# Kernel tuning notes

Hardware: AMD Instinct MI355X
Metric: run time of the kernel (lower is better)

## Reference

```python
import jax, jax.numpy as jnp
import numpy as np

N_NODES = 100000
N_EDGES = 1600000
IN_DIM = 128
HID = 128
OUT_DIM = 1
EPS = 1e-5
NEG_SLOPE = 0.01


def _glorot(key, shape):
    fan_in = shape[-1]
    return jax.random.normal(key, shape, dtype=jnp.float32) / np.sqrt(fan_in)


def setup_inputs() -> dict:
    key = jax.random.key(0)
    ks = jax.random.split(key, 16)
    x = jax.random.normal(ks[0], (N_NODES, IN_DIM), dtype=jnp.float32)
    edge_index = jax.random.randint(ks[1], (2, N_EDGES), 0, N_NODES, dtype=jnp.int64 if jax.config.jax_enable_x64 else jnp.int32)
    params = {
        'W_in': _glorot(ks[2], (HID, IN_DIM)), 'b_in': jnp.zeros((HID,), jnp.float32),
        # SAGEConv params: lin_l (applied to max-aggregated neighbors, with bias), lin_r (applied to self, no bias)
        'W_l1': _glorot(ks[3], (HID, HID)), 'b_l1': jnp.zeros((HID,), jnp.float32), 'W_r1': _glorot(ks[4], (HID, HID)),
        'W_l2': _glorot(ks[5], (HID, HID)), 'b_l2': jnp.zeros((HID,), jnp.float32), 'W_r2': _glorot(ks[6], (HID, HID)),
        'W_l3': _glorot(ks[7], (HID, HID)), 'b_l3': jnp.zeros((HID,), jnp.float32), 'W_r3': _glorot(ks[8], (HID, HID)),
        'g1': jnp.ones((HID,), jnp.float32), 'be1': jnp.zeros((HID,), jnp.float32),
        'g2': jnp.ones((HID,), jnp.float32), 'be2': jnp.zeros((HID,), jnp.float32),
        'g3': jnp.ones((HID,), jnp.float32), 'be3': jnp.zeros((HID,), jnp.float32),
        'W_fc1': _glorot(ks[9], (HID // 2, HID)), 'b_fc1': jnp.zeros((HID // 2,), jnp.float32),
        'W_fc2': _glorot(ks[10], (OUT_DIM, HID // 2)), 'b_fc2': jnp.zeros((OUT_DIM,), jnp.float32),
    }
    return {'x': x, 'edge_index': edge_index, **params}


def _sage_conv_max(x, src, dst, W_l, b_l, W_r):
    # gather source features per edge, scatter-max into destination nodes
    agg = jax.ops.segment_max(x[src], dst, num_segments=N_NODES)  # [N, H], -inf where no neighbors
    agg = jnp.where(jnp.isfinite(agg), agg, 0.0)
    return agg @ W_l.T + b_l + x @ W_r.T


def _batch_norm(x, gamma, beta):
    mean = x.mean(axis=0)
    var = x.var(axis=0)
    return gamma * (x - mean) * jax.lax.rsqrt(var + EPS) + beta


def _lrelu(x):
    return jax.nn.leaky_relu(x, negative_slope=NEG_SLOPE)


def reference(x, edge_index, W_in, b_in,
              W_l1, b_l1, W_r1, W_l2, b_l2, W_r2, W_l3, b_l3, W_r3,
              g1, be1, g2, be2, g3, be3,
              W_fc1, b_fc1, W_fc2, b_fc2):
    src, dst = edge_index[0], edge_index[1]
    h = x @ W_in.T + b_in
    residual = h
    h = _lrelu(_batch_norm(_sage_conv_max(h, src, dst, W_l1, b_l1, W_r1), g1, be1))
    h = _lrelu(_batch_norm(_sage_conv_max(h, src, dst, W_l2, b_l2, W_r2), g2, be2))
    h = _lrelu(_batch_norm(_sage_conv_max(h, src, dst, W_l3, b_l3, W_r3), g3, be3))
    h = h + residual  # dropout layers are identity in deterministic/eval reference
    h = _lrelu(h @ W_fc1.T + b_fc1)
    return h @ W_fc2.T + b_fc2  # [N, OUT_DIM]
```

## Files before the change

kernel.cpp:

```cpp
#include <hip/hip_runtime.h>
#include <cstdint>
#include <cstddef>

#define HID 128

typedef __bf16 bf16x8 __attribute__((ext_vector_type(8)));
typedef float f32x4 __attribute__((ext_vector_type(4)));

__device__ __forceinline__ float bf2f(uint32_t u) {
    union { uint32_t i; float f; } x; x.i = u << 16; return x.f;
}
__device__ __forceinline__ float bflo(uint32_t p) { return bf2f(p & 0xffffu); }
__device__ __forceinline__ float bfhi(uint32_t p) { return bf2f(p >> 16); }
__device__ __forceinline__ float bfs(const uint16_t* p) { return bf2f((uint32_t)*p); }
__device__ __forceinline__ uint16_t f2bf(float f) {
    union { float f; uint32_t i; } x; x.f = f;
    uint32_t u = x.i;
    return (uint16_t)((u + 0x7fffu + ((u >> 16) & 1u)) >> 16);
}
__device__ __forceinline__ uint32_t pack2(float a, float b) {
    return (uint32_t)f2bf(a) | ((uint32_t)f2bf(b) << 16);
}
__device__ __forceinline__ float lrelu_f(float v) { return v > 0.f ? v : 0.01f * v; }
__device__ __forceinline__ bf16x8 ldfrag(const uint16_t* p) {
    union { uint4 u; bf16x8 b; } c;
    c.u = *(const uint4*)p;
    return c.b;
}

__global__ __launch_bounds__(256) void sentinel_kernel(float* out, int n) {
    int i = blockIdx.x * 256 + threadIdx.x;
    if (i < n) out[i] = 65536.0f;
}

__global__ void detect_e_kernel(const int* __restrict__ ei, int* __restrict__ flagE) {
    int lane = threadIdx.x;
    int w = ei[2 * lane + 1];
    unsigned long long b = __ballot(w != 0);
    if (lane == 0) flagE[0] = (b == 0ULL) ? 1 : 0;
}
__global__ void detect_f_kernel(const uint32_t* __restrict__ x, int* __restrict__ flagF) {
    int lane = threadIdx.x;
    uint32_t e = (x[lane] >> 7) & 0xFFu;
    unsigned long long b = __ballot(e >= 64u && e <= 144u);
    if (lane == 0) flagF[0] = (b == ~0ULL) ? 0 : 1;
}

struct WArgs {
    const void* src[8];
    uint16_t* dst[8];
    int nrows[8];
};
__global__ __launch_bounds__(256) void convert_w(WArgs a, const int* __restrict__ flagF) {
    int mat = blockIdx.x >> 6;
    int idx = ((blockIdx.x & 63) << 8) + threadIdx.x;
    if (idx < a.nrows[mat] * HID) {
        a.dst[mat][idx] = flagF[0] ? f2bf(((const float*)a.src[mat])[idx])
                                   : ((const uint16_t*)a.src[mat])[idx];
    }
}

struct ParamArgs {
    const void* src[14];
    int off[14];
    int cnt[14];
};
__global__ __launch_bounds__(128) void convert_params(ParamArgs pa, float* __restrict__ params,
                                                      const int* __restrict__ flagF) {
    int b = blockIdx.x, t = threadIdx.x;
    if (t < pa.cnt[b]) {
        float v = flagF[0] ? ((const float*)pa.src[b])[t]
                           : bfs(&((const uint16_t*)pa.src[b])[t]);
        params[pa.off[b] + t] = v;
    }
}

__global__ __launch_bounds__(256) void convert_x(const void* __restrict__ x,
                                                 uint32_t* __restrict__ dst,
                                                 const int* __restrict__ flagF, int total2) {
    int i = blockIdx.x * 256 + threadIdx.x;
    if (i >= total2) return;
    if (flagF[0]) {
        float2 v = ((const float2*)x)[i];
        dst[i] = pack2(v.x, v.y);
    } else {
        dst[i] = ((const uint32_t*)x)[i];
    }
}

#define EPB 2048

__global__ __launch_bounds__(256) void bucket_hist(const int* __restrict__ ei,
                                                   const int* __restrict__ flagE,
                                                   int* __restrict__ bcnt, int E, int NBC) {
    __shared__ int cnt[1024];
    int tid = threadIdx.x;
    for (int b = tid; b < NBC; b += 256) cnt[b] = 0;
    __syncthreads();
    int e0 = blockIdx.x * EPB, e1 = min(e0 + EPB, E);
    int isl = flagE[0];
    for (int i = e0 + tid; i < e1; i += 256) {
        int d = isl ? ei[2 * (E + i)] : ei[E + i];
        atomicAdd(&cnt[d >> 10], 1);
    }
    __syncthreads();
    for (int b = tid; b < NBC; b += 256)
        if (cnt[b]) atomicAdd(&bcnt[b], cnt[b]);
}
__global__ __launch_bounds__(1024) void bucket_scan(const int* __restrict__ bcnt,
                                                    int* __restrict__ bstart,
                                                    int* __restrict__ gcur, int NBC, int E) {
    __shared__ int sm[1024];
    int tid = threadIdx.x;
    int v = (tid < NBC) ? bcnt[tid] : 0;
    sm[tid] = v;
    __syncthreads();
    for (int off = 1; off < 1024; off <<= 1) {
        int t = (tid >= off) ? sm[tid - off] : 0;
        __syncthreads();
        sm[tid] += t;
        __syncthreads();
    }
    int ex = sm[tid] - v;
    if (tid < NBC) { bstart[tid] = ex; gcur[tid] = ex; }
    if (tid == 0) bstart[NBC] = E;
}
__global__ __launch_bounds__(256) void bucket_fill(const int* __restrict__ ei,
                                                   const int* __restrict__ flagE,
                                                   int* __restrict__ gcur,
                                                   uint2* __restrict__ bins, int E, int NBC) {
    __shared__ int cnt[1024];
    __shared__ int res[1024];
    int tid = threadIdx.x;
    for (int b = tid; b < NBC; b += 256) cnt[b] = 0;
    __syncthreads();
    int e0 = blockIdx.x * EPB, e1 = min(e0 + EPB, E);
    int isl = flagE[0];
    for (int i = e0 + tid; i < e1; i += 256) {
        int d = isl ? ei[2 * (E + i)] : ei[E + i];
        atomicAdd(&cnt[d >> 10], 1);
    }
    __syncthreads();
    for (int b = tid; b < NBC; b += 256) {
        res[b] = cnt[b] ? atomicAdd(&gcur[b], cnt[b]) : 0;
        cnt[b] = 0;
    }
    __syncthreads();
    for (int i = e0 + tid; i < e1; i += 256) {
        int s = isl ? ei[2 * i] : ei[i];
        int d = isl ? ei[2 * (E + i)] : ei[E + i];
        int b = d >> 10;
        int pos = res[b] + atomicAdd(&cnt[b], 1);
        bins[pos] = make_uint2((uint32_t)s, (uint32_t)d);
    }
}
__global__ __launch_bounds__(256) void csr_build(const uint2* __restrict__ bins,
                                                 const int* __restrict__ bstart,
                                                 int* __restrict__ rowptr,
                                                 int* __restrict__ csr, int M, int E) {
    int b = blockIdx.x;
    int node0 = b << 10;
    int nn = min(1024, M - node0);
    int s = bstart[b], e = bstart[b + 1];
    __shared__ int cnt[1024];
    __shared__ int ofs[1024];
    int tid = threadIdx.x;
    for (int j = tid; j < 1024; j += 256) cnt[j] = 0;
    __syncthreads();
    for (int i = s + tid; i < e; i += 256)
        atomicAdd(&cnt[bins[i].y & 1023], 1);
    __syncthreads();
    if (tid == 0) {
        int run = s;
        for (int j = 0; j < nn; ++j) { ofs[j] = run; run += cnt[j]; }
    }
    __syncthreads();
    for (int j = tid; j < nn; j += 256) rowptr[node0 + j] = ofs[j];
    if (b == 0 && tid == 0) rowptr[M] = E;
    for (int j = tid; j < 1024; j += 256) cnt[j] = 0;
    __syncthreads();
    for (int i = s + tid; i < e; i += 256) {
        uint2 pr = bins[i];
        int d = pr.y & 1023;
        int pos = ofs[d] + atomicAdd(&cnt[d], 1);
        csr[pos] = (int)pr.x;
    }
}

__global__ __launch_bounds__(256) void gather_kernel(const uint4* __restrict__ cur,
                                                     const int* __restrict__ rowptr,
                                                     const int* __restrict__ csr,
                                                     uint4* __restrict__ agg, int M) {
    int gid = blockIdx.x * 256 + threadIdx.x;
    int node = gid >> 4;
    int sl = threadIdx.x & 15;
    if (node >= M) return;
    int b = rowptr[node], e = rowptr[node + 1];
    float m[8];
#pragma unroll
    for (int j = 0; j < 8; ++j) m[j] = -INFINITY;
    int i = b;
    for (; i + 4 <= e; i += 4) {
        int s0 = csr[i], s1 = csr[i + 1], s2 = csr[i + 2], s3 = csr[i + 3];
        uint4 u0 = cur[(size_t)s0 * 16 + sl];
        uint4 u1 = cur[(size_t)s1 * 16 + sl];
        uint4 u2 = cur[(size_t)s2 * 16 + sl];
        uint4 u3 = cur[(size_t)s3 * 16 + sl];
        uint32_t w0[4] = {u0.x, u0.y, u0.z, u0.w};
        uint32_t w1[4] = {u1.x, u1.y, u1.z, u1.w};
        uint32_t w2[4] = {u2.x, u2.y, u2.z, u2.w};
        uint32_t w3[4] = {u3.x, u3.y, u3.z, u3.w};
#pragma unroll
        for (int j = 0; j < 4; ++j) {
            float a0 = fmaxf(bflo(w0[j]), bflo(w1[j]));
            float a1 = fmaxf(bflo(w2[j]), bflo(w3[j]));
            float b0 = fmaxf(bfhi(w0[j]), bfhi(w1[j]));
            float b1 = fmaxf(bfhi(w2[j]), bfhi(w3[j]));
            m[2 * j]     = fmaxf(m[2 * j],     fmaxf(a0, a1));
            m[2 * j + 1] = fmaxf(m[2 * j + 1], fmaxf(b0, b1));
        }
    }
    for (; i < e; ++i) {
        int s0 = csr[i];
        uint4 u0 = cur[(size_t)s0 * 16 + sl];
        uint32_t w0[4] = {u0.x, u0.y, u0.z, u0.w};
#pragma unroll
        for (int j = 0; j < 4; ++j) {
            m[2 * j]     = fmaxf(m[2 * j],     bflo(w0[j]));
            m[2 * j + 1] = fmaxf(m[2 * j + 1], bfhi(w0[j]));
        }
    }
    if (b == e) {
#pragma unroll
        for (int j = 0; j < 8; ++j) m[j] = 0.f;
    }
    uint4 o;
    o.x = pack2(m[0], m[1]); o.y = pack2(m[2], m[3]);
    o.z = pack2(m[4], m[5]); o.w = pack2(m[6], m[7]);
    agg[(size_t)node * 16 + sl] = o;
}

template<int N, int NSRC, bool FC2>
__global__ __launch_bounds__(256, 3) void gemm_mfma(
    const uint16_t* __restrict__ A0, const uint16_t* __restrict__ W0,
    const uint16_t* __restrict__ A1, const uint16_t* __restrict__ W1,
    const float* __restrict__ bias, void* __restrict__ out_, int M,
    const float* __restrict__ fc2w)
{
    constexpr int LDT = 72;
    constexpr int WAVES_N = N / 64;
    constexpr int WAVES_M = 4 / WAVES_N;
    constexpr int MT = 8 / WAVES_M;
    constexpr int NT = 4;
    constexpr int NW = N / 32;
    constexpr int CHUNKS = 2 * NSRC;
    __shared__ uint16_t LX[128 * LDT];
    __shared__ uint16_t LW[N * LDT];
    const int tid = threadIdx.x;
    const int wave = tid >> 6, lane = tid & 63;
    const int l15 = lane & 15, lkg = lane >> 4;
    const int wn = (wave % WAVES_N) * 64;
    const int wm = (wave / WAVES_N) * (128 / WAVES_M);
    const int row0 = blockIdx.x * 128;
    const int srow = tid >> 3;
    const int sko = (tid & 7) * 8;

    f32x4 acc[NT][MT];
#pragma unroll
    for (int nt = 0; nt < NT; ++nt)
#pragma unroll
        for (int mt = 0; mt < MT; ++mt) {
            f32x4 z4 = {0.f, 0.f, 0.f, 0.f};
            acc[nt][mt] = z4;
        }

    const uint16_t* Asrc[2] = {A0, NSRC > 1 ? A1 : A0};
    const uint16_t* Wsrc[2] = {W0, NSRC > 1 ? W1 : W0};

    uint4 rx[4], rw[NW];
#pragma unroll
    for (int it = 0; it < 4; ++it) {
        int gr = row0 + srow + it * 32;
        uint4 v = make_uint4(0, 0, 0, 0);
        if (gr < M) v = *(const uint4*)(Asrc[0] + (size_t)gr * HID + sko);
        rx[it] = v;
    }
#pragma unroll
    for (int it = 0; it < NW; ++it)
        rw[it] = *(const uint4*)(Wsrc[0] + (size_t)(srow + it * 32) * HID + sko);

#pragma unroll 1
    for (int c = 0; c < CHUNKS; ++c) {
        __syncthreads();
#pragma unroll
        for (int it = 0; it < 4; ++it)
            *(uint4*)&LX[(srow + it * 32) * LDT + sko] = rx[it];
#pragma unroll
        for (int it = 0; it < NW; ++it)
            *(uint4*)&LW[(srow + it * 32) * LDT + sko] = rw[it];
        __syncthreads();
        if (c + 1 < CHUNKS) {
            int nc = c + 1, src = nc >> 1, kc = nc & 1;
            const uint16_t* Ag = Asrc[src];
#pragma unroll
            for (int it = 0; it < 4; ++it) {
                int gr = row0 + srow + it * 32;
                uint4 v = make_uint4(0, 0, 0, 0);
                if (gr < M) v = *(const uint4*)(Ag + (size_t)gr * HID + kc * 64 + sko);
                rx[it] = v;
            }
            const uint16_t* Wg = Wsrc[src];
#pragma unroll
            for (int it = 0; it < NW; ++it)
                rw[it] = *(const uint4*)(Wg + (size_t)(srow + it * 32) * HID + kc * 64 + sko);
        }
#pragma unroll
        for (int ks = 0; ks < 2; ++ks) {
            bf16x8 xf[MT], wf[NT];
#pragma unroll
            for (int mt = 0; mt < MT; ++mt)
                xf[mt] = ldfrag(&LX[(wm + mt * 16 + l15) * LDT + ks * 32 + lkg * 8]);
#pragma unroll
            for (int nt = 0; nt < NT; ++nt)
                wf[nt] = ldfrag(&LW[(wn + nt * 16 + l15) * LDT + ks * 32 + lkg * 8]);
#pragma unroll
            for (int nt = 0; nt < NT; ++nt)
#pragma unroll
                for (int mt = 0; mt < MT; ++mt)
                    acc[nt][mt] = __builtin_amdgcn_mfma_f32_16x16x32_bf16(
                        wf[nt], xf[mt], acc[nt][mt], 0, 0, 0);
        }
    }

    if constexpr (FC2) {
        float rowdot[MT];
#pragma unroll
        for (int mt = 0; mt < MT; ++mt) rowdot[mt] = 0.f;
#pragma unroll
        for (int nt = 0; nt < NT; ++nt) {
            int n0 = wn + nt * 16 + lkg * 4;
            float b4[4] = {bias[n0], bias[n0 + 1], bias[n0 + 2], bias[n0 + 3]};
            float w4[4] = {fc2w[n0], fc2w[n0 + 1], fc2w[n0 + 2], fc2w[n0 + 3]};
#pragma unroll
            for (int mt = 0; mt < MT; ++mt) {
                f32x4 f = acc[nt][mt];
#pragma unroll
                for (int j = 0; j < 4; ++j)
                    rowdot[mt] = fmaf(lrelu_f(f[j] + b4[j]), w4[j], rowdot[mt]);
            }
        }
        float b2 = fc2w[64];
#pragma unroll
        for (int mt = 0; mt < MT; ++mt) {
            float v = rowdot[mt];
            v += __shfl_xor(v, 16, 64);
            v += __shfl_xor(v, 32, 64);
            int m = row0 + wm + mt * 16 + l15;
            if (lkg == 0 && m < M) ((float*)out_)[m] = v + b2;
        }
    } else {
#pragma unroll
        for (int nt = 0; nt < NT; ++nt) {
            int n0 = wn + nt * 16 + lkg * 4;
            float b0 = bias[n0], b1 = bias[n0 + 1], b2 = bias[n0 + 2], b3 = bias[n0 + 3];
#pragma unroll
            for (int mt = 0; mt < MT; ++mt) {
                int m = row0 + wm + mt * 16 + l15;
                if (m < M) {
                    f32x4 f = acc[nt][mt];
                    ushort4 ov;
                    ov.x = f2bf(f[0] + b0); ov.y = f2bf(f[1] + b1);
                    ov.z = f2bf(f[2] + b2); ov.w = f2bf(f[3] + b3);
                    *(ushort4*)((uint16_t*)out_ + (size_t)m * N + n0) = ov;
                }
            }
        }
    }
}

__global__ __launch_bounds__(256) void bn_stats(const uint32_t* __restrict__ z,
                                                float* __restrict__ stats, int M, int rpb) {
    __shared__ float4 red[256];
    int c2 = threadIdx.x & 63;
    int part = threadIdx.x >> 6;
    int s0 = blockIdx.x * rpb, e0 = min(s0 + rpb, M);
    float sl = 0.f, s2l = 0.f, sh = 0.f, s2h = 0.f;
    for (int r = s0 + part; r < e0; r += 4) {
        uint32_t u = z[(size_t)r * 64 + c2];
        float a = bflo(u), b = bfhi(u);
        sl += a; s2l = fmaf(a, a, s2l);
        sh += b; s2h = fmaf(b, b, s2h);
    }
    red[threadIdx.x] = make_float4(sl, s2l, sh, s2h);
    __syncthreads();
    if (threadIdx.x < 64) {
        float4 v = red[threadIdx.x];
        float4 v1 = red[threadIdx.x + 64], v2 = red[threadIdx.x + 128], v3 = red[threadIdx.x + 192];
        v.x += v1.x + v2.x + v3.x; v.y += v1.y + v2.y + v3.y;
        v.z += v1.z + v2.z + v3.z; v.w += v1.w + v2.w + v3.w;
        int cc = c2 * 2;
        atomicAdd(&stats[cc], v.x);
        atomicAdd(&stats[128 + cc], v.y);
        atomicAdd(&stats[cc + 1], v.z);
        atomicAdd(&stats[129 + cc], v.w);
    }
}
__global__ void bn_finalize(float* stats, const float* __restrict__ g,
                            const float* __restrict__ be, int M) {
    int c = threadIdx.x;
    float mean = stats[c] / (float)M;
    float var = stats[128 + c] / (float)M - mean * mean;
    float sc = g[c] * rsqrtf(var + 1e-5f);
    stats[c] = sc;
    stats[128 + c] = be[c] - mean * sc;
}
__global__ __launch_bounds__(256) void bn_apply(uint32_t* __restrict__ z,
                                                const float* __restrict__ stats, int total2) {
    int i = blockIdx.x * 256 + threadIdx.x;
    if (i >= total2) return;
    int cc = (i & 63) * 2;
    uint32_t u = z[i];
    float a = lrelu_f(fmaf(bflo(u), stats[cc], stats[128 + cc]));
    float b = lrelu_f(fmaf(bfhi(u), stats[cc + 1], stats[129 + cc]));
    z[i] = pack2(a, b);
}
__global__ __launch_bounds__(256) void bn_apply_res(uint32_t* __restrict__ z,
                                                    const uint32_t* __restrict__ h0,
                                                    const float* __restrict__ stats, int total2) {
    int i = blockIdx.x * 256 + threadIdx.x;
    if (i >= total2) return;
    int cc = (i & 63) * 2;
    uint32_t u = z[i], r = h0[i];
    float a = lrelu_f(fmaf(bflo(u), stats[cc], stats[128 + cc])) + bflo(r);
    float b = lrelu_f(fmaf(bfhi(u), stats[cc + 1], stats[129 + cc])) + bfhi(r);
    z[i] = pack2(a, b);
}

extern "C" void kernel_launch(void* const* d_in, const int* in_sizes, int n_in,
                              void* d_out, int out_size, void* d_ws, size_t ws_size,
                              hipStream_t stream) {
    const void* x = d_in[0];
    const int* ei = (const int*)d_in[1];
    const int M = in_sizes[0] / HID;
    const int E = in_sizes[1] / 2;
    const int NBC = (M + 1023) >> 10;

    const size_t FEAT = (size_t)M * HID * 2;
    char* p = (char*)d_ws;
    uint16_t* H0 = (uint16_t*)p; p += FEAT;
    uint16_t* P  = (uint16_t*)p; p += FEAT;
    uint16_t* Q  = (uint16_t*)p; p += FEAT;
    uint16_t* WT = (uint16_t*)p; p += 8 * 16384 * 2;
    float* params = (float*)p; p += 8192;
    int* rowptr  = (int*)p; p += ((size_t)M + 32) * 4;
    int* csr     = (int*)p; p += (size_t)E * 4;
    int* bcnt    = (int*)p; p += 1024 * 4;
    int* bstart  = (int*)p; p += 1056 * 4;
    int* gcur    = (int*)p; p += 1024 * 4;
    float* stats = (float*)p; p += 3 * 256 * 4;
    int* flagE   = (int*)p; p += 128;
    int* flagF   = (int*)p; p += 128;

    const size_t needed = (size_t)(p - (char*)d_ws);
    if (needed > ws_size) {
        sentinel_kernel<<<(out_size + 255) / 256, 256, 0, stream>>>(
            (float*)d_out, out_size);
        return;
    }

    uint16_t* wt[8];
    for (int i = 0; i < 8; ++i) wt[i] = WT + (size_t)i * 16384;

    detect_e_kernel<<<1, 64, 0, stream>>>(ei, flagE);
    detect_f_kernel<<<1, 64, 0, stream>>>((const uint32_t*)x, flagF);

    WArgs wa;
    const int widx[8] = {2, 4, 6, 7, 9, 10, 12, 19};
    for (int i = 0; i < 8; ++i) {
        wa.src[i] = d_in[widx[i]];
        wa.dst[i] = wt[i];
        wa.nrows[i] = (i == 7) ? 64 : 128;
    }
    convert_w<<<512, 256, 0, stream>>>(wa, flagF);

    ParamArgs pa;
    const int pidx[14] = {3, 5, 8, 11, 13, 15, 17, 14, 16, 18, 20, 21, 22, 22};
    const int poff[14] = {0, 128, 256, 384, 512, 640, 768, 896, 1024, 1152, 1280, 1344, 1408, 1409};
    const int pcnt[14] = {128, 128, 128, 128, 128, 128, 128, 128, 128, 128, 64, 64, 1, 0};
    for (int i = 0; i < 14; ++i) { pa.src[i] = d_in[pidx[i]]; pa.off[i] = poff[i]; pa.cnt[i] = pcnt[i]; }
    convert_params<<<14, 128, 0, stream>>>(pa, params, flagF);

    const int total2 = M * (HID / 2);
    const int ew_grid = (total2 + 255) / 256;
    convert_x<<<ew_grid, 256, 0, stream>>>(x, (uint32_t*)Q, flagF, total2);

    hipMemsetAsync(bcnt, 0, 1024 * sizeof(int), stream);
    hipMemsetAsync(stats, 0, 3 * 256 * sizeof(float), stream);
    const int fgrid = (E + EPB - 1) / EPB;
    bucket_hist<<<fgrid, 256, 0, stream>>>(ei, flagE, bcnt, E, NBC);
    bucket_scan<<<1, 1024, 0, stream>>>(bcnt, bstart, gcur, NBC, E);
    bucket_fill<<<fgrid, 256, 0, stream>>>(ei, flagE, gcur, (uint2*)P, E, NBC);
    csr_build<<<NBC, 256, 0, stream>>>((const uint2*)P, bstart, rowptr, csr, M, E);

    const int gemm_grid = (M + 127) / 128;
    const int gather_grid = (M + 15) / 16;
    const int rpb = (M + 255) / 256;

    gemm_mfma<128, 1, false><<<gemm_grid, 256, 0, stream>>>(
        Q, wt[0], nullptr, nullptr, params + 0, H0, M, nullptr);

    uint16_t* wtl[3] = {wt[1], wt[3], wt[5]};
    uint16_t* wtr[3] = {wt[2], wt[4], wt[6]};
    uint16_t* cur = H0;
    uint16_t* dstb[3] = {P, Q, P};
    for (int l = 0; l < 3; ++l) {
        uint16_t* z = dstb[l];
        float* sl = stats + 256 * l;
        gather_kernel<<<gather_grid, 256, 0, stream>>>(
            (const uint4*)cur, rowptr, csr, (uint4*)z, M);
        gemm_mfma<128, 2, false><<<gemm_grid, 256, 0, stream>>>(
            z, wtl[l], cur, wtr[l], params + 128 + l * 128, z, M, nullptr);
        bn_stats<<<256, 256, 0, stream>>>((const uint32_t*)z, sl, M, rpb);
        bn_finalize<<<1, 128, 0, stream>>>(sl, params + 512 + l * 128,
                                           params + 896 + l * 128, M);
        if (l < 2)
            bn_apply<<<ew_grid, 256, 0, stream>>>((uint32_t*)z, sl, total2);
        else
            bn_apply_res<<<ew_grid, 256, 0, stream>>>((uint32_t*)z, (const uint32_t*)H0,
                                                      sl, total2);
        cur = z;
    }

    gemm_mfma<64, 1, true><<<gemm_grid, 256, 0, stream>>>(
        P, wt[7], nullptr, nullptr, params + 1280, (float*)d_out, M, params + 1344);
}
```

Baseline: 739.3 us.

## Fuse batch-norm statistics into SAGE GEMM epilogue and deepen gather unroll

The SAGE layer GEMM epilogue now computes per-column sums and sums of squares. It reduces them across lanes and waves and writes one partial per block. A small reduce_finalize kernel combines these partials and produces the scale/shift, replacing the separate bn_stats pass over the full feature matrix, the atomics and the stats memset. The gather kernel also issues eight neighbor loads per iteration to raise memory-level parallelism. The cost is that statistics are taken from fp32 values before bf16 rounding, which changes numerics slightly, and the GEMM epilogue gains register pressure and extra syncs.

Result: slower. 769.7 us (+4.1%).

```diff
diff --git a/kernel.cpp b/kernel.cpp
--- a/kernel.cpp
+++ b/kernel.cpp
@@ -200,29 +200,36 @@
 #pragma unroll
     for (int j = 0; j < 8; ++j) m[j] = -INFINITY;
     int i = b;
+    for (; i + 8 <= e; i += 8) {
+        uint4 u[8];
+#pragma unroll
+        for (int t = 0; t < 8; ++t) u[t] = cur[(size_t)csr[i + t] * 16 + sl];
+#pragma unroll
+        for (int t = 0; t < 8; ++t) {
+            uint32_t w[4] = {u[t].x, u[t].y, u[t].z, u[t].w};
+#pragma unroll
+            for (int j = 0; j < 4; ++j) {
+                m[2 * j]     = fmaxf(m[2 * j],     bflo(w[j]));
+                m[2 * j + 1] = fmaxf(m[2 * j + 1], bfhi(w[j]));
+            }
+        }
+    }
     for (; i + 4 <= e; i += 4) {
-        int s0 = csr[i], s1 = csr[i + 1], s2 = csr[i + 2], s3 = csr[i + 3];
-        uint4 u0 = cur[(size_t)s0 * 16 + sl];
-        uint4 u1 = cur[(size_t)s1 * 16 + sl];
-        uint4 u2 = cur[(size_t)s2 * 16 + sl];
-        uint4 u3 = cur[(size_t)s3 * 16 + sl];
-        uint32_t w0[4] = {u0.x, u0.y, u0.z, u0.w};
-        uint32_t w1[4] = {u1.x, u1.y, u1.z, u1.w};
-        uint32_t w2[4] = {u2.x, u2.y, u2.z, u2.w};
-        uint32_t w3[4] = {u3.x, u3.y, u3.z, u3.w};
-#pragma unroll
-        for (int j = 0; j < 4; ++j) {
-            float a0 = fmaxf(bflo(w0[j]), bflo(w1[j]));
-            float a1 = fmaxf(bflo(w2[j]), bflo(w3[j]));
-            float b0 = fmaxf(bfhi(w0[j]), bfhi(w1[j]));
-            float b1 = fmaxf(bfhi(w2[j]), bfhi(w3[j]));
-            m[2 * j]     = fmaxf(m[2 * j],     fmaxf(a0, a1));
-            m[2 * j + 1] = fmaxf(m[2 * j + 1], fmaxf(b0, b1));
+        uint4 u[4];
+#pragma unroll
+        for (int t = 0; t < 4; ++t) u[t] = cur[(size_t)csr[i + t] * 16 + sl];
+#pragma unroll
+        for (int t = 0; t < 4; ++t) {
+            uint32_t w[4] = {u[t].x, u[t].y, u[t].z, u[t].w};
+#pragma unroll
+            for (int j = 0; j < 4; ++j) {
+                m[2 * j]     = fmaxf(m[2 * j],     bflo(w[j]));
+                m[2 * j + 1] = fmaxf(m[2 * j + 1], bfhi(w[j]));
+            }
         }
     }
     for (; i < e; ++i) {
-        int s0 = csr[i];
-        uint4 u0 = cur[(size_t)s0 * 16 + sl];
+        uint4 u0 = cur[(size_t)csr[i] * 16 + sl];
         uint32_t w0[4] = {u0.x, u0.y, u0.z, u0.w};
 #pragma unroll
         for (int j = 0; j < 4; ++j) {
@@ -240,12 +247,12 @@
     agg[(size_t)node * 16 + sl] = o;
 }
 
-template<int N, int NSRC, bool FC2>
+template<int N, int NSRC, bool FC2, bool STATS>
 __global__ __launch_bounds__(256, 3) void gemm_mfma(
     const uint16_t* __restrict__ A0, const uint16_t* __restrict__ W0,
     const uint16_t* __restrict__ A1, const uint16_t* __restrict__ W1,
     const float* __restrict__ bias, void* __restrict__ out_, int M,
-    const float* __restrict__ fc2w)
+    const float* __restrict__ fc2w, float* __restrict__ pblk)
 {
     constexpr int LDT = 72;
     constexpr int WAVES_N = N / 64;
@@ -359,6 +366,11 @@
             if (lkg == 0 && m < M) ((float*)out_)[m] = v + b2;
         }
     } else {
+        float cs[16], cq[16];
+        if constexpr (STATS) {
+#pragma unroll
+            for (int v = 0; v < 16; ++v) { cs[v] = 0.f; cq[v] = 0.f; }
+        }
 #pragma unroll
         for (int nt = 0; nt < NT; ++nt) {
             int n0 = wn + nt * 16 + lkg * 4;
@@ -368,52 +380,74 @@
                 int m = row0 + wm + mt * 16 + l15;
                 if (m < M) {
                     f32x4 f = acc[nt][mt];
+                    float o0 = f[0] + b0, o1 = f[1] + b1, o2 = f[2] + b2, o3 = f[3] + b3;
+                    if constexpr (STATS) {
+                        cs[nt * 4 + 0] += o0; cq[nt * 4 + 0] = fmaf(o0, o0, cq[nt * 4 + 0]);
+                        cs[nt * 4 + 1] += o1; cq[nt * 4 + 1] = fmaf(o1, o1, cq[nt * 4 + 1]);
+                        cs[nt * 4 + 2] += o2; cq[nt * 4 + 2] = fmaf(o2, o2, cq[nt * 4 + 2]);
+                        cs[nt * 4 + 3] += o3; cq[nt * 4 + 3] = fmaf(o3, o3, cq[nt * 4 + 3]);
+                    }
                     ushort4 ov;
-                    ov.x = f2bf(f[0] + b0); ov.y = f2bf(f[1] + b1);
-                    ov.z = f2bf(f[2] + b2); ov.w = f2bf(f[3] + b3);
+                    ov.x = f2bf(o0); ov.y = f2bf(o1);
+                    ov.z = f2bf(o2); ov.w = f2bf(o3);
                     *(ushort4*)((uint16_t*)out_ + (size_t)m * N + n0) = ov;
                 }
             }
         }
-    }
-}
-
-__global__ __launch_bounds__(256) void bn_stats(const uint32_t* __restrict__ z,
-                                                float* __restrict__ stats, int M, int rpb) {
-    __shared__ float4 red[256];
-    int c2 = threadIdx.x & 63;
-    int part = threadIdx.x >> 6;
-    int s0 = blockIdx.x * rpb, e0 = min(s0 + rpb, M);
-    float sl = 0.f, s2l = 0.f, sh = 0.f, s2h = 0.f;
-    for (int r = s0 + part; r < e0; r += 4) {
-        uint32_t u = z[(size_t)r * 64 + c2];
-        float a = bflo(u), b = bfhi(u);
-        sl += a; s2l = fmaf(a, a, s2l);
-        sh += b; s2h = fmaf(b, b, s2h);
-    }
-    red[threadIdx.x] = make_float4(sl, s2l, sh, s2h);
-    __syncthreads();
-    if (threadIdx.x < 64) {
-        float4 v = red[threadIdx.x];
-        float4 v1 = red[threadIdx.x + 64], v2 = red[threadIdx.x + 128], v3 = red[threadIdx.x + 192];
-        v.x += v1.x + v2.x + v3.x; v.y += v1.y + v2.y + v3.y;
-        v.z += v1.z + v2.z + v3.z; v.w += v1.w + v2.w + v3.w;
-        int cc = c2 * 2;
-        atomicAdd(&stats[cc], v.x);
-        atomicAdd(&stats[128 + cc], v.y);
-        atomicAdd(&stats[cc + 1], v.z);
-        atomicAdd(&stats[129 + cc], v.w);
-    }
-}
-__global__ void bn_finalize(float* stats, const float* __restrict__ g,
-                            const float* __restrict__ be, int M) {
-    int c = threadIdx.x;
-    float mean = stats[c] / (float)M;
-    float var = stats[128 + c] / (float)M - mean * mean;
-    float sc = g[c] * rsqrtf(var + 1e-5f);
-    stats[c] = sc;
-    stats[128 + c] = be[c] - mean * sc;
-}
+        if constexpr (STATS) {
+#pragma unroll
+            for (int v = 0; v < 16; ++v) {
+                float a = cs[v], q = cq[v];
+                a += __shfl_xor(a, 1, 64); q += __shfl_xor(q, 1, 64);
+                a += __shfl_xor(a, 2, 64); q += __shfl_xor(q, 2, 64);
+                a += __shfl_xor(a, 4, 64); q += __shfl_xor(q, 4, 64);
+                a += __shfl_xor(a, 8, 64); q += __shfl_xor(q, 8, 64);
+                cs[v] = a; cq[v] = q;
+            }
+            float* sred = (float*)LX;
+            __syncthreads();
+            if (l15 == 0) {
+                int g = wave >> 1;
+#pragma unroll
+                for (int v = 0; v < 16; ++v) {
+                    int col = wn + (v >> 2) * 16 + lkg * 4 + (v & 3);
+                    sred[g * 256 + col] = cs[v];
+                    sred[g * 256 + 128 + col] = cq[v];
+                }
+            }
+            __syncthreads();
+            pblk[(size_t)blockIdx.x * 256 + tid] = sred[tid] + sred[256 + tid];
+        }
+    }
+}
+
+__global__ __launch_bounds__(256) void reduce_finalize(const float* __restrict__ pblk,
+                                                       int nblk, float* __restrict__ stats,
+                                                       const float* __restrict__ g,
+                                                       const float* __restrict__ be, int M) {
+    __shared__ float sm[2][256];
+    int tid = threadIdx.x;
+    int col = blockIdx.x * 16 + (tid & 15);
+    int chunk = tid >> 4;
+    float s = 0.f, q = 0.f;
+    for (int b = chunk; b < nblk; b += 16) {
+        s += pblk[(size_t)b * 256 + col];
+        q += pblk[(size_t)b * 256 + 128 + col];
+    }
+    sm[0][tid] = s; sm[1][tid] = q;
+    __syncthreads();
+    if (tid < 16) {
+        float s2 = 0.f, q2 = 0.f;
+        for (int j = 0; j < 16; ++j) { s2 += sm[0][tid + 16 * j]; q2 += sm[1][tid + 16 * j]; }
+        int c = blockIdx.x * 16 + tid;
+        float mean = s2 / (float)M;
+        float var = q2 / (float)M - mean * mean;
+        float sc = g[c] * rsqrtf(var + 1e-5f);
+        stats[c] = sc;
+        stats[128 + c] = be[c] - mean * sc;
+    }
+}
+
 __global__ __launch_bounds__(256) void bn_apply(uint32_t* __restrict__ z,
                                                 const float* __restrict__ stats, int total2) {
     int i = blockIdx.x * 256 + threadIdx.x;
@@ -444,6 +478,7 @@
     const int M = in_sizes[0] / HID;
     const int E = in_sizes[1] / 2;
     const int NBC = (M + 1023) >> 10;
+    const int gemm_grid = (M + 127) / 128;
 
     const size_t FEAT = (size_t)M * HID * 2;
     char* p = (char*)d_ws;
@@ -458,6 +493,7 @@
     int* bstart  = (int*)p; p += 1056 * 4;
     int* gcur    = (int*)p; p += 1024 * 4;
     float* stats = (float*)p; p += 3 * 256 * 4;
+    float* pblk  = (float*)p; p += (size_t)gemm_grid * 256 * 4;
     int* flagE   = (int*)p; p += 128;
     int* flagF   = (int*)p; p += 128;
 
@@ -495,19 +531,16 @@
     convert_x<<<ew_grid, 256, 0, stream>>>(x, (uint32_t*)Q, flagF, total2);
 
     hipMemsetAsync(bcnt, 0, 1024 * sizeof(int), stream);
-    hipMemsetAsync(stats, 0, 3 * 256 * sizeof(float), stream);
     const int fgrid = (E + EPB - 1) / EPB;
     bucket_hist<<<fgrid, 256, 0, stream>>>(ei, flagE, bcnt, E, NBC);
     bucket_scan<<<1, 1024, 0, stream>>>(bcnt, bstart, gcur, NBC, E);
     bucket_fill<<<fgrid, 256, 0, stream>>>(ei, flagE, gcur, (uint2*)P, E, NBC);
     csr_build<<<NBC, 256, 0, stream>>>((const uint2*)P, bstart, rowptr, csr, M, E);
 
-    const int gemm_grid = (M + 127) / 128;
     const int gather_grid = (M + 15) / 16;
-    const int rpb = (M + 255) / 256;
-
-    gemm_mfma<128, 1, false><<<gemm_grid, 256, 0, stream>>>(
-        Q, wt[0], nullptr, nullptr, params + 0, H0, M, nullptr);
+
+    gemm_mfma<128, 1, false, false><<<gemm_grid, 256, 0, stream>>>(
+        Q, wt[0], nullptr, nullptr, params + 0, H0, M, nullptr, nullptr);
 
     uint16_t* wtl[3] = {wt[1], wt[3], wt[5]};
     uint16_t* wtr[3] = {wt[2], wt[4], wt[6]};
@@ -518,11 +551,11 @@
         float* sl = stats + 256 * l;
         gather_kernel<<<gather_grid, 256, 0, stream>>>(
             (const uint4*)cur, rowptr, csr, (uint4*)z, M);
-        gemm_mfma<128, 2, false><<<gemm_grid, 256, 0, stream>>>(
-            z, wtl[l], cur, wtr[l], params + 128 + l * 128, z, M, nullptr);
-        bn_stats<<<256, 256, 0, stream>>>((const uint32_t*)z, sl, M, rpb);
-        bn_finalize<<<1, 128, 0, stream>>>(sl, params + 512 + l * 128,
-                                           params + 896 + l * 128, M);
+        gemm_mfma<128, 2, false, true><<<gemm_grid, 256, 0, stream>>>(
+            z, wtl[l], cur, wtr[l], params + 128 + l * 128, z, M, nullptr, pblk);
+        reduce_finalize<<<8, 256, 0, stream>>>(pblk, gemm_grid, sl,
+                                               params + 512 + l * 128,
+                                               params + 896 + l * 128, M);
         if (l < 2)
             bn_apply<<<ew_grid, 256, 0, stream>>>((uint32_t*)z, sl, total2);
         else
@@ -531,6 +564,7 @@
         cur = z;
     }
 
-    gemm_mfma<64, 1, true><<<gemm_grid, 256, 0, stream>>>(
-        P, wt[7], nullptr, nullptr, params + 1280, (float*)d_out, M, params + 1344);
-}
+    gemm_mfma<64, 1, true, false><<<gemm_grid, 256, 0, stream>>>(
+        P, wt[7], nullptr, nullptr, params + 1280, (float*)d_out, M,
+        params + 1344, nullptr);
+}
```
